# Performance work log

Measured on AMD Instinct MI355X. Metric: run time of the kernel, lower is better.

## Reference

```python
import jax, jax.numpy as jnp
import numpy as np

NUM_HEADS = 32
HEAD_DIM = 128  # 4096 / 32


def setup_inputs() -> dict:
    key = jax.random.key(0)
    k1, k2, k3 = jax.random.split(key, 3)
    B, S, H = 1, 2048, 4096
    hidden_states = jax.random.normal(k1, (B, S, H), dtype=jnp.float32)
    # causal additive mask, broadcast over heads: 0 on/below diagonal, large negative above
    neg = jnp.finfo(jnp.float32).min
    causal = jnp.triu(jnp.full((S, S), neg, dtype=jnp.float32), k=1)
    attention_mask = causal[None, None, :, :]  # [1,1,S,S]
    w_pack = jax.random.normal(k2, (3 * H, H), dtype=jnp.float32) * 0.02
    w_o = jax.random.normal(k3, (H, H), dtype=jnp.float32) * 0.02
    return {"hidden_states": hidden_states, "attention_mask": attention_mask,
            "w_pack": w_pack, "w_o": w_o}


def reference(hidden_states, attention_mask, w_pack, w_o):
    B, S, H = hidden_states.shape
    nh, hd = NUM_HEADS, HEAD_DIM
    # fused QKV projection (Linear, no bias): x @ W^T
    proj = hidden_states @ w_pack.T                      # [B,S,3H]
    q, k, v = jnp.split(proj, 3, axis=-1)
    q = q.reshape(B, S, nh, hd).transpose(0, 2, 1, 3)    # [B,nh,S,hd]
    k = k.reshape(B, S, nh, hd).transpose(0, 2, 1, 3)
    v = v.reshape(B, S, nh, hd).transpose(0, 2, 1, 3)
    scale = 1.0 / jnp.sqrt(jnp.float32(hd))
    attn = jnp.einsum('bhqd,bhkd->bhqk', q, k) * scale   # [B,nh,S,S]
    attn = attn + attention_mask
    attn = jnp.maximum(attn, jnp.finfo(attn.dtype).min)  # clamp like torch.max(..., finfo.min)
    attn = jax.nn.softmax(attn, axis=-1)
    out = jnp.einsum('bhqk,bhkd->bhqd', attn, v)         # [B,nh,S,hd]
    out = out.transpose(0, 2, 1, 3).reshape(B, S, nh * hd)
    return out @ w_o.T                                    # [B,S,H]
```

## Files before the change

### kernel.cpp

```cpp
#include <hip/hip_runtime.h>
#include <stdint.h>

typedef __attribute__((ext_vector_type(8))) short short8;
typedef __attribute__((ext_vector_type(4))) short short4v;
typedef __attribute__((ext_vector_type(4))) float floatx4;

#define SEQ    2048
#define HID    4096
#define NHEAD  32
#define HDIMV  128
#define PROJN  12288

__device__ __forceinline__ unsigned short f2bf(float f) {
  union { float f; unsigned u; } v; v.f = f;
  unsigned r = (v.u + 0x7fffu + ((v.u >> 16) & 1u)) >> 16;
  return (unsigned short)r;
}

__device__ __forceinline__ void g2l16(const void* g, void* l) {
  __builtin_amdgcn_global_load_lds(
      (const __attribute__((address_space(1))) void*)g,
      (__attribute__((address_space(3))) void*)l, 16, 0, 0);
}

__global__ __launch_bounds__(256) void pack_all(
    const float* __restrict__ hs, const float* __restrict__ wp,
    const float* __restrict__ wo,
    unsigned short* __restrict__ Ap1, unsigned short* __restrict__ Bp1,
    unsigned short* __restrict__ Bp2) {
  __shared__ __align__(16) unsigned short T[128 * 64];
  const int rp_g = blockIdx.x, kt = blockIdx.y, t = threadIdx.x;
  const float* src;
  unsigned short* dst;
  int rp;
  float sc;
  if (rp_g < 16) {
    src = hs; dst = Ap1; rp = rp_g; sc = 1.0f;
  } else if (rp_g < 112) {
    src = wp; dst = Bp1; rp = rp_g - 16;
    sc = (rp < 32) ? 0.12751744154f : 1.0f;
  } else {
    src = wo; dst = Bp2; rp = rp_g - 112; sc = 1.0f;
  }
  const long tb = ((long)rp * 64 + kt) * 8192;

#pragma unroll
  for (int pass = 0; pass < 8; pass++) {
    int r = pass * 16 + (t >> 4);
    int c4 = (t & 15) * 4;
    float4 a = *(const float4*)(src + (long)(rp * 128 + r) * HID + kt * 64 + c4);
    int chunk = (c4 >> 3) ^ (r & 7);
    short4v o;
    o[0] = (short)f2bf(a.x * sc); o[1] = (short)f2bf(a.y * sc);
    o[2] = (short)f2bf(a.z * sc); o[3] = (short)f2bf(a.w * sc);
    *(short4v*)(T + r * 64 + chunk * 8 + (c4 & 7)) = o;
  }
  __syncthreads();

#pragma unroll
  for (int j = 0; j < 4; j++) {
    int ch = t + j * 256;
    int r = ch & 127, cc = ch >> 7;
    short8 o = *(const short8*)(T + r * 64 + ((cc ^ (r & 7)) * 8));
    *(short8*)(dst + tb + ch * 8) = o;
  }
}

template<int OUT_F32>
__global__ __launch_bounds__(256, 5) void gemm_pk(
    const unsigned short* __restrict__ Ap,
    const unsigned short* __restrict__ Bp,
    void* __restrict__ C, int N, int K) {
  __shared__ __align__(16) unsigned short As[8192];
  __shared__ __align__(16) unsigned short Bs[8192];
  const int t = threadIdx.x;
  const int wave = t >> 6, lane = t & 63;
  const int bid = blockIdx.x;
  const int xcd = bid & 7;
  const int li = bid >> 3;
  const int mi = li & 15;
  const int ni = (li >> 4) * 8 + xcd;
  const int KT = K >> 6;
  const unsigned short* at = Ap + (long)mi * KT * 8192 + t * 8;
  const unsigned short* bt = Bp + (long)ni * KT * 8192 + t * 8;
  unsigned short* asl = As + wave * 512;
  unsigned short* bsl = Bs + wave * 512;

  const int mw = (wave >> 1) * 64;
  const int nw = (wave & 1) * 64;
  const int lq = lane & 15, lg = lane >> 4;

  floatx4 zero = {0.f, 0.f, 0.f, 0.f};
  floatx4 acc[4][4];
  for (int i = 0; i < 4; i++)
    for (int j = 0; j < 4; j++) acc[i][j] = zero;

  for (int kt = 0; kt < KT; kt++) {
    __syncthreads();
    const unsigned short* ak = at + (long)kt * 8192;
    const unsigned short* bk = bt + (long)kt * 8192;
#pragma unroll
    for (int j = 0; j < 4; j++) g2l16(ak + j * 2048, asl + j * 2048);
#pragma unroll
    for (int j = 0; j < 4; j++) g2l16(bk + j * 2048, bsl + j * 2048);
    __syncthreads();
#pragma unroll
    for (int kk = 0; kk < 2; kk++) {
      const int ch = (kk * 4 + lg) * 1024;
      short8 af[4], bfr[4];
#pragma unroll
      for (int i = 0; i < 4; i++)
        af[i] = *(const short8*)(As + ch + (mw + i * 16 + lq) * 8);
#pragma unroll
      for (int j = 0; j < 4; j++)
        bfr[j] = *(const short8*)(Bs + ch + (nw + j * 16 + lq) * 8);
#pragma unroll
      for (int i = 0; i < 4; i++)
#pragma unroll
        for (int j = 0; j < 4; j++)
          acc[i][j] = __builtin_amdgcn_mfma_f32_16x16x32_bf16(af[i], bfr[j], acc[i][j], 0, 0, 0);
    }
  }

  const int row0 = mi * 128 + mw + lg * 4;
  const int col0 = ni * 128 + nw + lq;
  if (OUT_F32) {
    float* Cf = (float*)C;
#pragma unroll
    for (int i = 0; i < 4; i++)
#pragma unroll
      for (int j = 0; j < 4; j++)
#pragma unroll
        for (int r = 0; r < 4; r++)
          Cf[(long)(row0 + i * 16 + r) * N + col0 + j * 16] = acc[i][j][r];
  } else {
    unsigned short* Cb = (unsigned short*)C;
#pragma unroll
    for (int i = 0; i < 4; i++)
#pragma unroll
      for (int j = 0; j < 4; j++)
#pragma unroll
        for (int r = 0; r < 4; r++)
          Cb[(long)(row0 + i * 16 + r) * N + col0 + j * 16] = f2bf(acc[i][j][r]);
  }
}

__global__ __launch_bounds__(256, 5) void gemm_qkv(
    const unsigned short* __restrict__ Ap,
    const unsigned short* __restrict__ Bp,
    unsigned short* __restrict__ Qf,
    unsigned short* __restrict__ Kf,
    unsigned short* __restrict__ Vf) {
  __shared__ __align__(16) unsigned short As[8192];
  __shared__ __align__(16) unsigned short Bs[8192];
  const int t = threadIdx.x;
  const int wave = t >> 6, lane = t & 63;
  const int bid = blockIdx.x;
  const int xcd = bid & 7;
  const int li = bid >> 3;
  const int mi = li & 15;
  const int ni = (li >> 4) * 8 + xcd;
  const int KT = HID >> 6;
  const unsigned short* at = Ap + (long)mi * KT * 8192 + t * 8;
  const unsigned short* bt = Bp + (long)ni * KT * 8192 + t * 8;
  unsigned short* asl = As + wave * 512;
  unsigned short* bsl = Bs + wave * 512;

  const int mw = (wave >> 1) * 64;
  const int nw = (wave & 1) * 64;
  const int lq = lane & 15, lg = lane >> 4;

  floatx4 zero = {0.f, 0.f, 0.f, 0.f};
  floatx4 acc[4][4];
  for (int i = 0; i < 4; i++)
    for (int j = 0; j < 4; j++) acc[i][j] = zero;

  for (int kt = 0; kt < KT; kt++) {
    __syncthreads();
    const unsigned short* ak = at + (long)kt * 8192;
    const unsigned short* bk = bt + (long)kt * 8192;
#pragma unroll
    for (int j = 0; j < 4; j++) g2l16(ak + j * 2048, asl + j * 2048);
#pragma unroll
    for (int j = 0; j < 4; j++) g2l16(bk + j * 2048, bsl + j * 2048);
    __syncthreads();
#pragma unroll
    for (int kk = 0; kk < 2; kk++) {
      const int ch = (kk * 4 + lg) * 1024;
      short8 af[4], bfr[4];
#pragma unroll
      for (int i = 0; i < 4; i++)
        af[i] = *(const short8*)(As + ch + (mw + i * 16 + lq) * 8);
#pragma unroll
      for (int j = 0; j < 4; j++)
        bfr[j] = *(const short8*)(Bs + ch + (nw + j * 16 + lq) * 8);
#pragma unroll
      for (int i = 0; i < 4; i++)
#pragma unroll
        for (int j = 0; j < 4; j++)
          acc[i][j] = __builtin_amdgcn_mfma_f32_16x16x32_bf16(af[i], bfr[j], acc[i][j], 0, 0, 0);
    }
  }

  const int sec = ni >> 5;
  const int h = ni & 31;
  unsigned short* dst =
      (sec == 0 ? Qf : (sec == 1 ? Kf : Vf)) + ((long)(h * 16 + mi)) * 16384;
  if (sec < 2) {
#pragma unroll
    for (int i = 0; i < 4; i++)
#pragma unroll
      for (int j = 0; j < 4; j++)
#pragma unroll
        for (int r = 0; r < 4; r++) {
          int row = mw + i * 16 + lg * 4 + r;
          int c = nw + j * 16 + lq;
          dst[((c >> 3) * 128 + row) * 8 + (c & 7)] = f2bf(acc[i][j][r]);
        }
  } else {
#pragma unroll
    for (int i = 0; i < 4; i++)
#pragma unroll
      for (int j = 0; j < 4; j++)
#pragma unroll
        for (int r = 0; r < 4; r++) {
          int s = mw + i * 16 + lg * 4 + r;
          int d = nw + j * 16 + lq;
          dst[((s >> 3) * 128 + d) * 8 + (s & 7)] = f2bf(acc[i][j][r]);
        }
  }
}

__device__ __forceinline__ void stage_tile(const unsigned short* g, unsigned short* lds,
                                           int wave, int lane) {
  const unsigned short* gp = g + wave * 4096 + lane * 8;
  unsigned short* lp = lds + wave * 4096;
#pragma unroll
  for (int j = 0; j < 8; j++) g2l16(gp + j * 512, lp + j * 512);
}

__global__ __launch_bounds__(256, 1) void attn_kernel(
    const unsigned short* __restrict__ Qf,
    const unsigned short* __restrict__ Kf,
    const unsigned short* __restrict__ Vf,
    unsigned short* __restrict__ aop) {
  __shared__ __align__(16) unsigned short Ks[2][16384];
  __shared__ __align__(16) unsigned short Vs[2][16384];
  __shared__ __align__(16) unsigned short Ps[16384];
  const int bx = blockIdx.x;
  const int h = bx & 31;
  const int qt = 15 - (bx >> 5);
  const int t = threadIdx.x, wave = t >> 6, lane = t & 63;
  const int lq = lane & 15, lg = lane >> 4;
  const int wOff = wave * 32;

  const unsigned short* qb = Qf + ((long)(h * 16 + qt)) * 16384;
  short8 qf[2][4];
#pragma unroll
  for (int i = 0; i < 2; i++)
#pragma unroll
    for (int kk = 0; kk < 4; kk++)
      qf[i][kk] = *(const short8*)(qb + ((kk * 4 + lg) * 128 + wOff + i * 16 + lq) * 8);

  float mraw[2][4], lsum[2][4];
  floatx4 zero = {0.f, 0.f, 0.f, 0.f};
  floatx4 o[2][8];
#pragma unroll
  for (int i = 0; i < 2; i++)
#pragma unroll
    for (int r = 0; r < 4; r++) { mraw[i][r] = -INFINITY; lsum[i][r] = 0.f; }
#pragma unroll
  for (int i = 0; i < 2; i++)
#pragma unroll
    for (int j = 0; j < 8; j++) o[i][j] = zero;

  const unsigned short* kb0 = Kf + ((long)h * 16) * 16384;
  const unsigned short* vb0 = Vf + ((long)h * 16) * 16384;
  stage_tile(kb0, Ks[0], wave, lane);
  stage_tile(vb0, Vs[0], wave, lane);

  for (int kv = 0; kv <= qt; kv++) {
    const int cur = kv & 1;
    const bool diag = (kv == qt);
    __syncthreads();
    if (!diag) {
      stage_tile(kb0 + (long)(kv + 1) * 16384, Ks[1 - cur], wave, lane);
      stage_tile(vb0 + (long)(kv + 1) * 16384, Vs[1 - cur], wave, lane);
    }

    floatx4 s[2][8];
#pragma unroll
    for (int i = 0; i < 2; i++)
#pragma unroll
      for (int j = 0; j < 8; j++) s[i][j] = zero;
#pragma unroll
    for (int kk = 0; kk < 4; kk++) {
      short8 bfr[8];
#pragma unroll
      for (int j = 0; j < 8; j++)
        bfr[j] = *(const short8*)(&Ks[cur][((kk * 4 + lg) * 128 + j * 16 + lq) * 8]);
#pragma unroll
      for (int i = 0; i < 2; i++)
#pragma unroll
        for (int j = 0; j < 8; j++)
          s[i][j] = __builtin_amdgcn_mfma_f32_16x16x32_bf16(qf[i][kk], bfr[j], s[i][j], 0, 0, 0);
    }

    if (diag) {
#pragma unroll
      for (int i = 0; i < 2; i++)
#pragma unroll
        for (int r = 0; r < 4; r++) {
          int qrow = qt * 128 + wOff + i * 16 + lg * 4 + r;
#pragma unroll
          for (int j = 0; j < 8; j++)
            if (kv * 128 + j * 16 + lq > qrow) s[i][j][r] = -INFINITY;
        }
    }

    float alpha_[2][4];
#pragma unroll
    for (int i = 0; i < 2; i++) {
#pragma unroll
      for (int r = 0; r < 4; r++) {
        float mx = s[i][0][r];
#pragma unroll
        for (int j = 1; j < 8; j++) mx = fmaxf(mx, s[i][j][r]);
#pragma unroll
        for (int d = 1; d < 16; d <<= 1) mx = fmaxf(mx, __shfl_xor(mx, d, 64));
        float mnew = fmaxf(mraw[i][r], mx);
        float al = exp2f(mraw[i][r] - mnew);
        float ps = 0.f;
#pragma unroll
        for (int j = 0; j < 8; j++) {
          float p = exp2f(s[i][j][r] - mnew);
          s[i][j][r] = p;
          ps += p;
        }
#pragma unroll
        for (int d = 1; d < 16; d <<= 1) ps += __shfl_xor(ps, d, 64);
        lsum[i][r] = lsum[i][r] * al + ps;
        mraw[i][r] = mnew;
        alpha_[i][r] = al;
      }
    }
#pragma unroll
    for (int i = 0; i < 2; i++)
#pragma unroll
      for (int j = 0; j < 8; j++)
#pragma unroll
        for (int r = 0; r < 4; r++) o[i][j][r] *= alpha_[i][r];

#pragma unroll
    for (int i = 0; i < 2; i++)
#pragma unroll
      for (int r = 0; r < 4; r++) {
        int prow = wOff + i * 16 + lg * 4 + r;
#pragma unroll
        for (int j = 0; j < 8; j++)
          Ps[((j * 2 + (lq >> 3)) * 128 + prow) * 8 + (lq & 7)] = f2bf(s[i][j][r]);
      }

#pragma unroll
    for (int kk = 0; kk < 4; kk++) {
      short8 pf[2], vf[8];
#pragma unroll
      for (int i = 0; i < 2; i++)
        pf[i] = *(const short8*)(Ps + ((kk * 4 + lg) * 128 + wOff + i * 16 + lq) * 8);
#pragma unroll
      for (int j = 0; j < 8; j++)
        vf[j] = *(const short8*)(&Vs[cur][((kk * 4 + lg) * 128 + j * 16 + lq) * 8]);
#pragma unroll
      for (int i = 0; i < 2; i++)
#pragma unroll
        for (int j = 0; j < 8; j++)
          o[i][j] = __builtin_amdgcn_mfma_f32_16x16x32_bf16(pf[i], vf[j], o[i][j], 0, 0, 0);
    }
  }

#pragma unroll
  for (int i = 0; i < 2; i++) {
    float inv[4];
#pragma unroll
    for (int r = 0; r < 4; r++) inv[r] = 1.0f / lsum[i][r];
#pragma unroll
    for (int r = 0; r < 4; r++) {
      int prow = wOff + i * 16 + lg * 4 + r;
#pragma unroll
      for (int j = 0; j < 8; j++)
        Ps[((j * 2 + (lq >> 3)) * 128 + prow) * 8 + (lq & 7)] = f2bf(o[i][j][r] * inv[r]);
    }
  }
#pragma unroll
  for (int it = 0; it < 8; it++) {
    int row_loc = it * 4 + (lane >> 4);
    int cc = lane & 15;
    short8 v = *(const short8*)(Ps + (cc * 128 + wOff + row_loc) * 8);
    long tb = ((long)qt * 64 + h * 2 + (cc >> 3)) * 8192;
    *(short8*)(aop + tb + ((cc & 7) * 128 + wOff + row_loc) * 8) = v;
  }
}

extern "C" void kernel_launch(void* const* d_in, const int* in_sizes, int n_in,
                              void* d_out, int out_size, void* d_ws, size_t ws_size,
                              hipStream_t stream) {
  (void)in_sizes; (void)n_in; (void)out_size;
  const float* hs = (const float*)d_in[0];
  const float* wp = (const float*)d_in[2];
  const float* wo = (const float*)d_in[3];
  float* out = (float*)d_out;
  char* ws = (char*)d_ws;

  unsigned short* Ap1 = (unsigned short*)(ws);
  unsigned short* Bp1 = (unsigned short*)(ws + 16777216);
  unsigned short* Bp2 = (unsigned short*)(ws + 117440512);
  unsigned short* Qf  = (unsigned short*)(ws + 150994944);
  unsigned short* Kf  = (unsigned short*)(ws + 167772160);
  unsigned short* Vf  = (unsigned short*)(ws + 184549376);
  unsigned short* aop = (unsigned short*)(ws + 201326592);
  if (ws_size < 218103808) return;

  pack_all<<<dim3(144, 64), 256, 0, stream>>>(hs, wp, wo, Ap1, Bp1, Bp2);

  gemm_qkv<<<1536, 256, 0, stream>>>(Ap1, Bp1, Qf, Kf, Vf);

  attn_kernel<<<512, 256, 0, stream>>>(Qf, Kf, Vf, aop);

  gemm_pk<1><<<512, 256, 0, stream>>>(aop, Bp2, (void*)out, HID, HID);
}
```

Before: 785.6 us.

## Halve attention KV tile to 64 keys for two blocks per CU

The attention kernel now processes 64-key tiles instead of 128, halving the K/V/P shared-memory buffers so two blocks can reside per CU (launch bounds raised to 2). Q-tile scheduling is reordered so the first half of blocks take long tiles and the rest short ones, and MFMA sections are wrapped in s_setprio raises. The epilogue reuses the K buffer for output staging because Ps shrank. The cost is twice as many loop iterations and barriers, and a risk of register pressure under the tighter launch bound.

```diff
diff --git a/kernel.cpp b/kernel.cpp
--- a/kernel.cpp
+++ b/kernel.cpp
@@ -231,25 +231,18 @@
   }
 }
 
-__device__ __forceinline__ void stage_tile(const unsigned short* g, unsigned short* lds,
-                                           int wave, int lane) {
-  const unsigned short* gp = g + wave * 4096 + lane * 8;
-  unsigned short* lp = lds + wave * 4096;
-#pragma unroll
-  for (int j = 0; j < 8; j++) g2l16(gp + j * 512, lp + j * 512);
-}
-
-__global__ __launch_bounds__(256, 1) void attn_kernel(
+__global__ __launch_bounds__(256, 2) void attn_kernel(
     const unsigned short* __restrict__ Qf,
     const unsigned short* __restrict__ Kf,
     const unsigned short* __restrict__ Vf,
     unsigned short* __restrict__ aop) {
-  __shared__ __align__(16) unsigned short Ks[2][16384];
-  __shared__ __align__(16) unsigned short Vs[2][16384];
-  __shared__ __align__(16) unsigned short Ps[16384];
+  __shared__ __align__(16) unsigned short Ks[2][8192];
+  __shared__ __align__(16) unsigned short Vs[2][8192];
+  __shared__ __align__(16) unsigned short Ps[8192];
   const int bx = blockIdx.x;
   const int h = bx & 31;
-  const int qt = 15 - (bx >> 5);
+  const int idx = bx >> 5;
+  const int qt = (idx < 8) ? (15 - idx) : (idx - 8);
   const int t = threadIdx.x, wave = t >> 6, lane = t & 63;
   const int lq = lane & 15, lg = lane >> 4;
   const int wOff = wave * 32;
@@ -276,45 +269,65 @@
 
   const unsigned short* kb0 = Kf + ((long)h * 16) * 16384;
   const unsigned short* vb0 = Vf + ((long)h * 16) * 16384;
-  stage_tile(kb0, Ks[0], wave, lane);
-  stage_tile(vb0, Vs[0], wave, lane);
-
-  for (int kv = 0; kv <= qt; kv++) {
-    const int cur = kv & 1;
-    const bool diag = (kv == qt);
+  const int nkv = 2 * qt + 2;
+
+  auto stageK = [&](int buf, int kvt) {
+    const unsigned short* g = kb0 + (long)(kvt >> 1) * 16384 + (kvt & 1) * 512;
+#pragma unroll
+    for (int j = 0; j < 4; j++) {
+      int run = wave * 4 + j;
+      g2l16(g + run * 1024 + lane * 8, &Ks[buf][run * 512 + lane * 8]);
+    }
+  };
+  auto stageV = [&](int buf, int kvt) {
+    const unsigned short* g = vb0 + (long)(kvt >> 1) * 16384 + (kvt & 1) * 8192;
+#pragma unroll
+    for (int j = 0; j < 4; j++) {
+      int run = wave * 4 + j;
+      g2l16(g + run * 512 + lane * 8, &Vs[buf][run * 512 + lane * 8]);
+    }
+  };
+
+  stageK(0, 0);
+  stageV(0, 0);
+
+  for (int kvt = 0; kvt < nkv; kvt++) {
+    const int cur = kvt & 1;
     __syncthreads();
-    if (!diag) {
-      stage_tile(kb0 + (long)(kv + 1) * 16384, Ks[1 - cur], wave, lane);
-      stage_tile(vb0 + (long)(kv + 1) * 16384, Vs[1 - cur], wave, lane);
-    }
-
-    floatx4 s[2][8];
+    if (kvt + 1 < nkv) {
+      stageK(1 - cur, kvt + 1);
+      stageV(1 - cur, kvt + 1);
+    }
+
+    floatx4 s[2][4];
 #pragma unroll
     for (int i = 0; i < 2; i++)
 #pragma unroll
-      for (int j = 0; j < 8; j++) s[i][j] = zero;
+      for (int j = 0; j < 4; j++) s[i][j] = zero;
 #pragma unroll
     for (int kk = 0; kk < 4; kk++) {
-      short8 bfr[8];
-#pragma unroll
-      for (int j = 0; j < 8; j++)
-        bfr[j] = *(const short8*)(&Ks[cur][((kk * 4 + lg) * 128 + j * 16 + lq) * 8]);
+      short8 bfr[4];
+#pragma unroll
+      for (int j = 0; j < 4; j++)
+        bfr[j] = *(const short8*)(&Ks[cur][((kk * 4 + lg) * 64 + j * 16 + lq) * 8]);
+      __builtin_amdgcn_s_setprio(1);
 #pragma unroll
       for (int i = 0; i < 2; i++)
 #pragma unroll
-        for (int j = 0; j < 8; j++)
+        for (int j = 0; j < 4; j++)
           s[i][j] = __builtin_amdgcn_mfma_f32_16x16x32_bf16(qf[i][kk], bfr[j], s[i][j], 0, 0, 0);
-    }
-
-    if (diag) {
+      __builtin_amdgcn_s_setprio(0);
+    }
+
+    if (kvt >= 2 * qt) {
 #pragma unroll
       for (int i = 0; i < 2; i++)
 #pragma unroll
         for (int r = 0; r < 4; r++) {
           int qrow = qt * 128 + wOff + i * 16 + lg * 4 + r;
 #pragma unroll
-          for (int j = 0; j < 8; j++)
-            if (kv * 128 + j * 16 + lq > qrow) s[i][j][r] = -INFINITY;
+          for (int j = 0; j < 4; j++)
+            if (kvt * 64 + j * 16 + lq > qrow) s[i][j][r] = -INFINITY;
         }
     }
 
@@ -325,14 +338,14 @@
       for (int r = 0; r < 4; r++) {
         float mx = s[i][0][r];
 #pragma unroll
-        for (int j = 1; j < 8; j++) mx = fmaxf(mx, s[i][j][r]);
+        for (int j = 1; j < 4; j++) mx = fmaxf(mx, s[i][j][r]);
 #pragma unroll
         for (int d = 1; d < 16; d <<= 1) mx = fmaxf(mx, __shfl_xor(mx, d, 64));
         float mnew = fmaxf(mraw[i][r], mx);
         float al = exp2f(mraw[i][r] - mnew);
         float ps = 0.f;
 #pragma unroll
-        for (int j = 0; j < 8; j++) {
+        for (int j = 0; j < 4; j++) {
           float p = exp2f(s[i][j][r] - mnew);
           s[i][j][r] = p;
           ps += p;
@@ -357,12 +370,12 @@
       for (int r = 0; r < 4; r++) {
         int prow = wOff + i * 16 + lg * 4 + r;
 #pragma unroll
-        for (int j = 0; j < 8; j++)
+        for (int j = 0; j < 4; j++)
           Ps[((j * 2 + (lq >> 3)) * 128 + prow) * 8 + (lq & 7)] = f2bf(s[i][j][r]);
       }
 
 #pragma unroll
-    for (int kk = 0; kk < 4; kk++) {
+    for (int kk = 0; kk < 2; kk++) {
       short8 pf[2], vf[8];
 #pragma unroll
       for (int i = 0; i < 2; i++)
@@ -370,14 +383,18 @@
 #pragma unroll
       for (int j = 0; j < 8; j++)
         vf[j] = *(const short8*)(&Vs[cur][((kk * 4 + lg) * 128 + j * 16 + lq) * 8]);
+      __builtin_amdgcn_s_setprio(1);
 #pragma unroll
       for (int i = 0; i < 2; i++)
 #pragma unroll
         for (int j = 0; j < 8; j++)
           o[i][j] = __builtin_amdgcn_mfma_f32_16x16x32_bf16(pf[i], vf[j], o[i][j], 0, 0, 0);
-    }
-  }
-
+      __builtin_amdgcn_s_setprio(0);
+    }
+  }
+
+  __syncthreads();
+  unsigned short* Es = &Ks[0][0];
 #pragma unroll
   for (int i = 0; i < 2; i++) {
     float inv[4];
@@ -388,14 +405,14 @@
       int prow = wOff + i * 16 + lg * 4 + r;
 #pragma unroll
       for (int j = 0; j < 8; j++)
-        Ps[((j * 2 + (lq >> 3)) * 128 + prow) * 8 + (lq & 7)] = f2bf(o[i][j][r] * inv[r]);
+        Es[((j * 2 + (lq >> 3)) * 128 + prow) * 8 + (lq & 7)] = f2bf(o[i][j][r] * inv[r]);
     }
   }
 #pragma unroll
   for (int it = 0; it < 8; it++) {
     int row_loc = it * 4 + (lane >> 4);
     int cc = lane & 15;
-    short8 v = *(const short8*)(Ps + (cc * 128 + wOff + row_loc) * 8);
+    short8 v = *(const short8*)(Es + (cc * 128 + wOff + row_loc) * 8);
     long tb = ((long)qt * 64 + h * 2 + (cc >> 3)) * 8192;
     *(short8*)(aop + tb + ((cc & 7) * 128 + wOff + row_loc) * 8) = v;
   }
```

After: 779.5 us. About the same (-0.8%).
